# Kernel optimization log

Measured on AMD Instinct MI355X. Metric: run time of the kernel, lower is better.

The kernel has to match this reference:

```python
import jax, jax.numpy as jnp
import numpy as np

N_NODES = 100000
N_EDGES = 3200000
IN_F, HID, OUT = 3, 32, 1
NEG_SLOPE = 0.2


def _glorot(key, shape):
    fan_in, fan_out = shape[0], shape[-1]
    lim = jnp.sqrt(6.0 / (fan_in + fan_out)).astype(jnp.float32)
    return jax.random.uniform(key, shape, jnp.float32, -lim, lim)


def setup_inputs() -> dict:
    key = jax.random.key(0)
    ks = jax.random.split(key, 12)
    x = jax.random.normal(ks[0], (N_NODES, IN_F), jnp.float32)
    edge_index = jax.random.randint(ks[1], (2, N_EDGES), 0, N_NODES, jnp.int32)
    return {
        "x": x,
        "edge_index": edge_index,
        "W1": _glorot(ks[2], (IN_F, HID)),
        "att_src1": _glorot(ks[3], (1, HID))[0],
        "att_dst1": _glorot(ks[4], (1, HID))[0],
        "b1": jnp.zeros((HID,), jnp.float32),
        "W2": _glorot(ks[5], (HID, HID)),
        "att_src2": _glorot(ks[6], (1, HID))[0],
        "att_dst2": _glorot(ks[7], (1, HID))[0],
        "b2": jnp.zeros((HID,), jnp.float32),
        "Wl": _glorot(ks[8], (HID, OUT)),
        "bl": jnp.zeros((OUT,), jnp.float32),
    }


def gat_layer(x, src, dst, W, att_src, att_dst, b):
    # h: [N, HID] dense transform
    h = x @ W
    # per-node attention halves (compute once per node, gather per edge)
    a_s = h @ att_src  # [N]
    a_d = h @ att_dst  # [N]
    logits = jax.nn.leaky_relu(a_s[src] + a_d[dst], NEG_SLOPE)  # [E+N]
    # segment-softmax over incoming edges of each dst node
    m = jax.ops.segment_max(logits, dst, num_segments=N_NODES)
    m = jnp.where(jnp.isfinite(m), m, 0.0)
    ex = jnp.exp(logits - m[dst])
    denom = jax.ops.segment_sum(ex, dst, num_segments=N_NODES)
    coef = ex / (denom[dst] + 1e-16)
    # weighted scatter-aggregate of source messages
    out = jax.ops.segment_sum(coef[:, None] * h[src], dst, num_segments=N_NODES)
    return out + b


def reference(x, edge_index, W1, att_src1, att_dst1, b1, W2, att_src2, att_dst2, b2, Wl, bl):
    # PyG GATConv default: add self-loops
    loops = jnp.arange(N_NODES, dtype=edge_index.dtype)
    src = jnp.concatenate([edge_index[0], loops])
    dst = jnp.concatenate([edge_index[1], loops])
    h = gat_layer(x, src, dst, W1, att_src1, att_dst1, b1)
    h = jax.nn.relu(h)  # dropout is identity in eval
    h = gat_layer(h, src, dst, W2, att_src2, att_dst2, b2)
    h = jax.nn.relu(h)
    return h @ Wl + bl
```

## Files before the change

kernel.cpp:

```cpp
#include <hip/hip_runtime.h>
#include <hip/hip_fp16.h>

#define HID 32
#define BN 98
#define NBPAD 1024
#define BSTRIDE 3584
#define CHUNK 6144
#define EPT 12
#define CPAD 16

__device__ __forceinline__ float lrelu(float x) { return x > 0.0f ? x : 0.2f * x; }


__global__ void k_transform1(const float* __restrict__ x,
                             const float* __restrict__ W1,
                             const float* __restrict__ att_src,
                             const float* __restrict__ att_dst,
                             __half* __restrict__ hh,
                             float* __restrict__ a_s,
                             float* __restrict__ a_d,
                             int* __restrict__ cursor, int N)
{
    int tid = blockIdx.x * blockDim.x + threadIdx.x;
    if (tid < NBPAD * CPAD) cursor[tid] = 0;
    int n = tid >> 5, f = tid & 31;
    if (n >= N) return;
    float x0 = x[n * 3 + 0], x1 = x[n * 3 + 1], x2 = x[n * 3 + 2];
    float hv = x0 * W1[f] + x1 * W1[HID + f] + x2 * W1[2 * HID + f];
    hh[(size_t)n * HID + f] = __float2half(hv);
    float as = hv * att_src[f];
    float ad = hv * att_dst[f];
    #pragma unroll
    for (int m = 16; m >= 1; m >>= 1) {
        as += __shfl_xor(as, m, 32);
        ad += __shfl_xor(ad, m, 32);
    }
    if (f == 0) { a_s[n] = as; a_d[n] = ad; }
}


struct BinSM {
    int stage[CHUNK];
    unsigned short sbid[CHUNK];
    int lhist[NBPAD], lexcl[NBPAD], lbase[NBPAD], lcur[NBPAD];
    int arr[256];
};

__global__ void __launch_bounds__(512) k_binscatter(const int* __restrict__ src,
        const int* __restrict__ dst, int* __restrict__ cursor,
        unsigned int* __restrict__ packed, int NBr, int E)
{
    __shared__ BinSM S;
    int t = threadIdx.x;
    int base = blockIdx.x * CHUNK;
    int cnt = E - base; if (cnt > CHUNK) cnt = CHUNK;

    for (int i = t; i < NBPAD; i += 512) { S.lhist[i] = 0; S.lcur[i] = 0; }
    __syncthreads();

    int myd[EPT], mys[EPT];
    #pragma unroll
    for (int u = 0; u < EPT; ++u) {
        int i = t + u * 512;
        myd[u] = -1;
        if (i < cnt) {
            myd[u] = __builtin_nontemporal_load(&dst[base + i]);
            mys[u] = __builtin_nontemporal_load(&src[base + i]);
        }
    }
    #pragma unroll
    for (int u = 0; u < EPT; ++u)
        if (myd[u] >= 0) atomicAdd(&S.lhist[myd[u] / BN], 1);
    __syncthreads();

    int b0 = 4 * t;
    int c0 = 0, c1 = 0, c2 = 0, c3 = 0, s = 0;
    if (t < 256) {
        c0 = S.lhist[b0]; c1 = S.lhist[b0 + 1];
        c2 = S.lhist[b0 + 2]; c3 = S.lhist[b0 + 3];
        s = c0 + c1 + c2 + c3;
        S.arr[t] = s;
    }
    __syncthreads();
    for (int o = 1; o < 256; o <<= 1) {
        int v = (t < 256 && t >= o) ? S.arr[t - o] : 0;
        __syncthreads();
        if (t < 256) S.arr[t] += v;
        __syncthreads();
    }
    if (t < 256) {
        int ex = S.arr[t] - s;
        int e0 = ex, e1 = ex + c0, e2 = e1 + c1, e3 = e2 + c2;
        S.lexcl[b0] = e0; S.lexcl[b0 + 1] = e1;
        S.lexcl[b0 + 2] = e2; S.lexcl[b0 + 3] = e3;
        for (int i = 0; i < c0; ++i) S.sbid[e0 + i] = (unsigned short)b0;
        for (int i = 0; i < c1; ++i) S.sbid[e1 + i] = (unsigned short)(b0 + 1);
        for (int i = 0; i < c2; ++i) S.sbid[e2 + i] = (unsigned short)(b0 + 2);
        for (int i = 0; i < c3; ++i) S.sbid[e3 + i] = (unsigned short)(b0 + 3);
    }
    for (int b = t; b < NBr; b += 512)
        if (S.lhist[b])
            S.lbase[b] = b * BSTRIDE + atomicAdd(&cursor[b * CPAD], S.lhist[b]);
    __syncthreads();

    #pragma unroll
    for (int u = 0; u < EPT; ++u) {
        if (myd[u] >= 0) {
            int d = myd[u];
            int b = d / BN;
            int dl = d - b * BN;
            int idx = S.lexcl[b] + atomicAdd(&S.lcur[b], 1);
            S.stage[idx] = (int)((unsigned)mys[u] | ((unsigned)dl << 17));
        }
    }
    __syncthreads();

    for (int i = t; i < cnt; i += 512) {
        int b = S.sbid[i];
        int gpos = S.lbase[b] + (i - S.lexcl[b]);
        if (gpos < (b + 1) * BSTRIDE)
            __builtin_nontemporal_store((unsigned)S.stage[i], &packed[gpos]);
    }
}


struct AggSM {
    int2  lpair[BSTRIDE];
    int   lhist[256], lscan[256], lcur[256];
    float adT[BN];
};

__device__ __forceinline__ void build_csr(AggSM& S,
        const unsigned int* __restrict__ pk, int cnt,
        const float* __restrict__ a_s, const float* __restrict__ a_d,
        int nodeBase, int N)
{
    int t = threadIdx.x;
    if (t < 256) { S.lhist[t] = 0; S.lcur[t] = 0; }
    if (t < BN) { int n = nodeBase + t; S.adT[t] = (n < N) ? a_d[n] : 0.0f; }
    __syncthreads();
    unsigned myw[8];
    int mc = 0;
    for (int i = t; i < cnt; i += 512) {
        unsigned p = __builtin_nontemporal_load(&pk[i]);
        myw[mc++] = p;
        atomicAdd(&S.lhist[(p >> 17) & 255], 1);
    }
    __syncthreads();
    if (t < 256) S.lscan[t] = S.lhist[t];
    __syncthreads();
    for (int o = 1; o < 256; o <<= 1) {
        int v = (t < 256 && t >= o) ? S.lscan[t - o] : 0;
        __syncthreads();
        if (t < 256) S.lscan[t] += v;
        __syncthreads();
    }
    mc = 0;
    for (int i = t; i < cnt; i += 512) {
        unsigned p = myw[mc++];
        int dl = (p >> 17) & 255;
        int sv = (int)(p & 0x1FFFF);
        float e = __expf(lrelu(a_s[sv] + S.adT[dl]));
        int pos = atomicAdd(&S.lcur[dl], 1);
        S.lpair[(S.lscan[dl] - S.lhist[dl]) + pos] = make_int2(sv, __float_as_int(e));
    }
    __syncthreads();
}

__device__ __forceinline__ void agg_node(const __half* __restrict__ hh,
                                         float ex_self, const float* __restrict__ b,
                                         int n, int f,
                                         const int2* lpair,
                                         int off, int dg, float& vx, float& vy)
{
    float den = ex_self;
    float2 hs = __half22float2(*(const __half2*)(hh + (size_t)n * HID + 2 * f));
    float accx = ex_self * hs.x;
    float accy = ex_self * hs.y;
    int j = 0;
    for (; j + 8 <= dg; j += 8) {
        int2 p0 = lpair[off + j + 0], p1 = lpair[off + j + 1];
        int2 p2 = lpair[off + j + 2], p3 = lpair[off + j + 3];
        int2 p4 = lpair[off + j + 4], p5 = lpair[off + j + 5];
        int2 p6 = lpair[off + j + 6], p7 = lpair[off + j + 7];
        __half2 h0 = *(const __half2*)(hh + (size_t)p0.x * HID + 2 * f);
        __half2 h1 = *(const __half2*)(hh + (size_t)p1.x * HID + 2 * f);
        __half2 h2 = *(const __half2*)(hh + (size_t)p2.x * HID + 2 * f);
        __half2 h3 = *(const __half2*)(hh + (size_t)p3.x * HID + 2 * f);
        __half2 h4 = *(const __half2*)(hh + (size_t)p4.x * HID + 2 * f);
        __half2 h5 = *(const __half2*)(hh + (size_t)p5.x * HID + 2 * f);
        __half2 h6 = *(const __half2*)(hh + (size_t)p6.x * HID + 2 * f);
        __half2 h7 = *(const __half2*)(hh + (size_t)p7.x * HID + 2 * f);
        float e0 = __int_as_float(p0.y), e1 = __int_as_float(p1.y);
        float e2 = __int_as_float(p2.y), e3 = __int_as_float(p3.y);
        float e4 = __int_as_float(p4.y), e5 = __int_as_float(p5.y);
        float e6 = __int_as_float(p6.y), e7 = __int_as_float(p7.y);
        float2 q0 = __half22float2(h0), q1 = __half22float2(h1);
        float2 q2 = __half22float2(h2), q3 = __half22float2(h3);
        float2 q4 = __half22float2(h4), q5 = __half22float2(h5);
        float2 q6 = __half22float2(h6), q7 = __half22float2(h7);
        den += ((e0 + e1) + (e2 + e3)) + ((e4 + e5) + (e6 + e7));
        accx = fmaf(e0, q0.x, accx); accy = fmaf(e0, q0.y, accy);
        accx = fmaf(e1, q1.x, accx); accy = fmaf(e1, q1.y, accy);
        accx = fmaf(e2, q2.x, accx); accy = fmaf(e2, q2.y, accy);
        accx = fmaf(e3, q3.x, accx); accy = fmaf(e3, q3.y, accy);
        accx = fmaf(e4, q4.x, accx); accy = fmaf(e4, q4.y, accy);
        accx = fmaf(e5, q5.x, accx); accy = fmaf(e5, q5.y, accy);
        accx = fmaf(e6, q6.x, accx); accy = fmaf(e6, q6.y, accy);
        accx = fmaf(e7, q7.x, accx); accy = fmaf(e7, q7.y, accy);
    }
    for (; j < dg; ++j) {
        int2 p0 = lpair[off + j];
        float e0 = __int_as_float(p0.y);
        float2 q0 = __half22float2(*(const __half2*)(hh + (size_t)p0.x * HID + 2 * f));
        den += e0;
        accx = fmaf(e0, q0.x, accx);
        accy = fmaf(e0, q0.y, accy);
    }
    float inv = 1.0f / (den + 1e-16f);
    vx = fmaxf(accx * inv + b[2 * f], 0.0f);
    vy = fmaxf(accy * inv + b[2 * f + 1], 0.0f);
}

__device__ __forceinline__ void epi_mid(int n, int f, float vx, float vy,
        const float* __restrict__ W2, const float* __restrict__ as2w,
        const float* __restrict__ ad2w,
        __half* __restrict__ hh_out, float* __restrict__ as_out,
        float* __restrict__ ad_out)
{
    float hx = 0.0f, hy = 0.0f;
    #pragma unroll
    for (int k = 0; k < 16; ++k) {
        float va = __shfl(vx, k, 16);
        float vb = __shfl(vy, k, 16);
        float2 w0 = *(const float2*)(W2 + (2 * k) * HID + 2 * f);
        float2 w1 = *(const float2*)(W2 + (2 * k + 1) * HID + 2 * f);
        hx = fmaf(va, w0.x, hx); hy = fmaf(va, w0.y, hy);
        hx = fmaf(vb, w1.x, hx); hy = fmaf(vb, w1.y, hy);
    }
    *(__half2*)(hh_out + (size_t)n * HID + 2 * f) = __floats2half2_rn(hx, hy);
    float as = hx * as2w[2 * f] + hy * as2w[2 * f + 1];
    float ad = hx * ad2w[2 * f] + hy * ad2w[2 * f + 1];
    #pragma unroll
    for (int m2 = 8; m2 >= 1; m2 >>= 1) {
        as += __shfl_xor(as, m2, 16);
        ad += __shfl_xor(ad, m2, 16);
    }
    if (f == 0) { as_out[n] = as; ad_out[n] = ad; }
}


__global__ void __launch_bounds__(512, 8) k_agg_mid(const __half* __restrict__ hh,
        const float* __restrict__ a_s, const float* __restrict__ a_d,
        const int* __restrict__ cursor, const unsigned int* __restrict__ packed,
        const float* __restrict__ b1, const float* __restrict__ W2,
        const float* __restrict__ as2w, const float* __restrict__ ad2w,
        __half* __restrict__ hh_out, float* __restrict__ as_out,
        float* __restrict__ ad_out, int N)
{
    __shared__ AggSM S;
    int bk = blockIdx.x, t = threadIdx.x;
    int cnt = cursor[bk * CPAD]; if (cnt > BSTRIDE) cnt = BSTRIDE;
    build_csr(S, packed + (size_t)bk * BSTRIDE, cnt, a_s, a_d, bk * BN, N);
    int g = t >> 4, f = t & 15;
    for (int dl = g; dl < BN; dl += 32) {
        int n = bk * BN + dl;
        if (n >= N) continue;
        int off = S.lscan[dl] - S.lhist[dl];
        int dg = S.lhist[dl];
        float exs = __expf(lrelu(a_s[n] + S.adT[dl]));
        float vx, vy;
        agg_node(hh, exs, b1, n, f, S.lpair, off, dg, vx, vy);
        epi_mid(n, f, vx, vy, W2, as2w, ad2w, hh_out, as_out, ad_out);
    }
}

__global__ void __launch_bounds__(512, 8) k_agg_out(const __half* __restrict__ hh,
        const float* __restrict__ a_s, const float* __restrict__ a_d,
        const int* __restrict__ cursor, const unsigned int* __restrict__ packed,
        const float* __restrict__ b2, const float* __restrict__ Wl,
        const float* __restrict__ bl, float* __restrict__ out, int N)
{
    __shared__ AggSM S;
    int bk = blockIdx.x, t = threadIdx.x;
    int cnt = cursor[bk * CPAD]; if (cnt > BSTRIDE) cnt = BSTRIDE;
    build_csr(S, packed + (size_t)bk * BSTRIDE, cnt, a_s, a_d, bk * BN, N);
    int g = t >> 4, f = t & 15;
    for (int dl = g; dl < BN; dl += 32) {
        int n = bk * BN + dl;
        if (n >= N) continue;
        int off = S.lscan[dl] - S.lhist[dl];
        int dg = S.lhist[dl];
        float exs = __expf(lrelu(a_s[n] + S.adT[dl]));
        float vx, vy;
        agg_node(hh, exs, b2, n, f, S.lpair, off, dg, vx, vy);
        float y = vx * Wl[2 * f] + vy * Wl[2 * f + 1];
        #pragma unroll
        for (int m2 = 8; m2 >= 1; m2 >>= 1)
            y += __shfl_xor(y, m2, 16);
        if (f == 0) out[n] = y + bl[0];
    }
}


extern "C" void kernel_launch(void* const* d_in, const int* in_sizes, int n_in,
                              void* d_out, int out_size, void* d_ws, size_t ws_size,
                              hipStream_t stream)
{
    const float* x        = (const float*)d_in[0];
    const int*   eidx     = (const int*)d_in[1];
    const float* W1       = (const float*)d_in[2];
    const float* att_src1 = (const float*)d_in[3];
    const float* att_dst1 = (const float*)d_in[4];
    const float* b1       = (const float*)d_in[5];
    const float* W2       = (const float*)d_in[6];
    const float* att_src2 = (const float*)d_in[7];
    const float* att_dst2 = (const float*)d_in[8];
    const float* b2       = (const float*)d_in[9];
    const float* Wl       = (const float*)d_in[10];
    const float* bl       = (const float*)d_in[11];
    float* out = (float*)d_out;

    int N = in_sizes[0] / 3;
    int E = in_sizes[1] / 2;
    const int* src = eidx;
    const int* dst = eidx + E;
    int NBr = (N + BN - 1) / BN;

    size_t szNHh = (size_t)N * HID * 2;
    size_t szN4  = (size_t)N * 4;
    size_t szPK  = (size_t)NBr * BSTRIDE * 4;

    char* ws = (char*)d_ws;
    __half* h1h    = (__half*)ws; ws += szNHh;
    __half* h2h    = (__half*)ws; ws += szNHh;
    unsigned int* packed = (unsigned int*)ws; ws += szPK;
    float*  a_s1   = (float*)ws;  ws += szN4;
    float*  a_d1   = (float*)ws;  ws += szN4;
    float*  a_s2   = (float*)ws;  ws += szN4;
    float*  a_d2   = (float*)ws;  ws += szN4;
    int*    cursor = (int*)ws;    ws += (size_t)NBPAD * CPAD * 4;

    const int B = 256;
    int gridNode32 = (N * HID + B - 1) / B;
    int gridBin    = (E + CHUNK - 1) / CHUNK;

    k_transform1<<<gridNode32, B, 0, stream>>>(x, W1, att_src1, att_dst1,
                                               h1h, a_s1, a_d1, cursor, N);
    k_binscatter<<<gridBin, 512, 0, stream>>>(src, dst, cursor, packed, NBr, E);
    k_agg_mid<<<NBr, 512, 0, stream>>>(h1h, a_s1, a_d1, cursor, packed,
                                       b1, W2, att_src2, att_dst2,
                                       h2h, a_s2, a_d2, N);
    k_agg_out<<<NBr, 512, 0, stream>>>(h2h, a_s2, a_d2, cursor, packed,
                                       b2, Wl, bl, out, N);
}
```

Before: 270.0 us.

## Split node features into two half-width planes and gather each in separate passes

Node feature storage is split from one 32-wide fp16 row into two 16-wide planes (low and high feature halves). Aggregation now runs two passes over each node's edges, gathering 32 bytes per source from one plane at a time, so each pass touches a working set half the size, which is meant to fit better in cache. The cost is reading the edge list twice, plus scalar half loads in place of half2 loads. Separately, the nontemporal load/store hints in the bin scatter are dropped.

```diff
diff --git a/kernel.cpp b/kernel.cpp
--- a/kernel.cpp
+++ b/kernel.cpp
@@ -2,6 +2,7 @@
 #include <hip/hip_fp16.h>
 
 #define HID 32
+#define HHALF 16
 #define BN 98
 #define NBPAD 1024
 #define BSTRIDE 3584
@@ -16,7 +17,8 @@
                              const float* __restrict__ W1,
                              const float* __restrict__ att_src,
                              const float* __restrict__ att_dst,
-                             __half* __restrict__ hh,
+                             __half* __restrict__ h_lo,
+                             __half* __restrict__ h_hi,
                              float* __restrict__ a_s,
                              float* __restrict__ a_d,
                              int* __restrict__ cursor, int N)
@@ -27,7 +29,8 @@
     if (n >= N) return;
     float x0 = x[n * 3 + 0], x1 = x[n * 3 + 1], x2 = x[n * 3 + 2];
     float hv = x0 * W1[f] + x1 * W1[HID + f] + x2 * W1[2 * HID + f];
-    hh[(size_t)n * HID + f] = __float2half(hv);
+    if (f < HHALF) h_lo[(size_t)n * HHALF + f] = __float2half(hv);
+    else           h_hi[(size_t)n * HHALF + (f - HHALF)] = __float2half(hv);
     float as = hv * att_src[f];
     float ad = hv * att_dst[f];
     #pragma unroll
@@ -63,10 +66,7 @@
     for (int u = 0; u < EPT; ++u) {
         int i = t + u * 512;
         myd[u] = -1;
-        if (i < cnt) {
-            myd[u] = __builtin_nontemporal_load(&dst[base + i]);
-            mys[u] = __builtin_nontemporal_load(&src[base + i]);
-        }
+        if (i < cnt) { myd[u] = dst[base + i]; mys[u] = src[base + i]; }
     }
     #pragma unroll
     for (int u = 0; u < EPT; ++u)
@@ -119,7 +119,7 @@
         int b = S.sbid[i];
         int gpos = S.lbase[b] + (i - S.lexcl[b]);
         if (gpos < (b + 1) * BSTRIDE)
-            __builtin_nontemporal_store((unsigned)S.stage[i], &packed[gpos]);
+            packed[gpos] = (unsigned)S.stage[i];
     }
 }
 
@@ -167,80 +167,72 @@
     __syncthreads();
 }
 
-__device__ __forceinline__ void agg_node(const __half* __restrict__ hh,
-                                         float ex_self, const float* __restrict__ b,
-                                         int n, int f,
-                                         const int2* lpair,
-                                         int off, int dg, float& vx, float& vy)
-{
-    float den = ex_self;
-    float2 hs = __half22float2(*(const __half2*)(hh + (size_t)n * HID + 2 * f));
-    float accx = ex_self * hs.x;
-    float accy = ex_self * hs.y;
+template<bool WITH_DEN>
+__device__ __forceinline__ void agg_half(const __half* __restrict__ hh,
+        float exs, int n, int f, const int2* lpair, int off, int dg,
+        float& accOut, float& denOut)
+{
+    float den = exs;
+    float acc = exs * __half2float(hh[(size_t)n * HHALF + f]);
     int j = 0;
     for (; j + 8 <= dg; j += 8) {
         int2 p0 = lpair[off + j + 0], p1 = lpair[off + j + 1];
         int2 p2 = lpair[off + j + 2], p3 = lpair[off + j + 3];
         int2 p4 = lpair[off + j + 4], p5 = lpair[off + j + 5];
         int2 p6 = lpair[off + j + 6], p7 = lpair[off + j + 7];
-        __half2 h0 = *(const __half2*)(hh + (size_t)p0.x * HID + 2 * f);
-        __half2 h1 = *(const __half2*)(hh + (size_t)p1.x * HID + 2 * f);
-        __half2 h2 = *(const __half2*)(hh + (size_t)p2.x * HID + 2 * f);
-        __half2 h3 = *(const __half2*)(hh + (size_t)p3.x * HID + 2 * f);
-        __half2 h4 = *(const __half2*)(hh + (size_t)p4.x * HID + 2 * f);
-        __half2 h5 = *(const __half2*)(hh + (size_t)p5.x * HID + 2 * f);
-        __half2 h6 = *(const __half2*)(hh + (size_t)p6.x * HID + 2 * f);
-        __half2 h7 = *(const __half2*)(hh + (size_t)p7.x * HID + 2 * f);
+        __half v0 = hh[(size_t)p0.x * HHALF + f];
+        __half v1 = hh[(size_t)p1.x * HHALF + f];
+        __half v2 = hh[(size_t)p2.x * HHALF + f];
+        __half v3 = hh[(size_t)p3.x * HHALF + f];
+        __half v4 = hh[(size_t)p4.x * HHALF + f];
+        __half v5 = hh[(size_t)p5.x * HHALF + f];
+        __half v6 = hh[(size_t)p6.x * HHALF + f];
+        __half v7 = hh[(size_t)p7.x * HHALF + f];
         float e0 = __int_as_float(p0.y), e1 = __int_as_float(p1.y);
         float e2 = __int_as_float(p2.y), e3 = __int_as_float(p3.y);
         float e4 = __int_as_float(p4.y), e5 = __int_as_float(p5.y);
         float e6 = __int_as_float(p6.y), e7 = __int_as_float(p7.y);
-        float2 q0 = __half22float2(h0), q1 = __half22float2(h1);
-        float2 q2 = __half22float2(h2), q3 = __half22float2(h3);
-        float2 q4 = __half22float2(h4), q5 = __half22float2(h5);
-        float2 q6 = __half22float2(h6), q7 = __half22float2(h7);
-        den += ((e0 + e1) + (e2 + e3)) + ((e4 + e5) + (e6 + e7));
-        accx = fmaf(e0, q0.x, accx); accy = fmaf(e0, q0.y, accy);
-        accx = fmaf(e1, q1.x, accx); accy = fmaf(e1, q1.y, accy);
-        accx = fmaf(e2, q2.x, accx); accy = fmaf(e2, q2.y, accy);
-        accx = fmaf(e3, q3.x, accx); accy = fmaf(e3, q3.y, accy);
-        accx = fmaf(e4, q4.x, accx); accy = fmaf(e4, q4.y, accy);
-        accx = fmaf(e5, q5.x, accx); accy = fmaf(e5, q5.y, accy);
-        accx = fmaf(e6, q6.x, accx); accy = fmaf(e6, q6.y, accy);
-        accx = fmaf(e7, q7.x, accx); accy = fmaf(e7, q7.y, accy);
+        if (WITH_DEN)
+            den += ((e0 + e1) + (e2 + e3)) + ((e4 + e5) + (e6 + e7));
+        acc = fmaf(e0, __half2float(v0), acc);
+        acc = fmaf(e1, __half2float(v1), acc);
+        acc = fmaf(e2, __half2float(v2), acc);
+        acc = fmaf(e3, __half2float(v3), acc);
+        acc = fmaf(e4, __half2float(v4), acc);
+        acc = fmaf(e5, __half2float(v5), acc);
+        acc = fmaf(e6, __half2float(v6), acc);
+        acc = fmaf(e7, __half2float(v7), acc);
     }
     for (; j < dg; ++j) {
-        int2 p0 = lpair[off + j];
-        float e0 = __int_as_float(p0.y);
-        float2 q0 = __half22float2(*(const __half2*)(hh + (size_t)p0.x * HID + 2 * f));
-        den += e0;
-        accx = fmaf(e0, q0.x, accx);
-        accy = fmaf(e0, q0.y, accy);
-    }
-    float inv = 1.0f / (den + 1e-16f);
-    vx = fmaxf(accx * inv + b[2 * f], 0.0f);
-    vy = fmaxf(accy * inv + b[2 * f + 1], 0.0f);
+        int2 pp = lpair[off + j];
+        float e = __int_as_float(pp.y);
+        if (WITH_DEN) den += e;
+        acc = fmaf(e, __half2float(hh[(size_t)pp.x * HHALF + f]), acc);
+    }
+    accOut = acc;
+    if (WITH_DEN) denOut = den;
 }
 
 __device__ __forceinline__ void epi_mid(int n, int f, float vx, float vy,
         const float* __restrict__ W2, const float* __restrict__ as2w,
         const float* __restrict__ ad2w,
-        __half* __restrict__ hh_out, float* __restrict__ as_out,
-        float* __restrict__ ad_out)
+        __half* __restrict__ h2_lo, __half* __restrict__ h2_hi,
+        float* __restrict__ as_out, float* __restrict__ ad_out)
 {
     float hx = 0.0f, hy = 0.0f;
     #pragma unroll
     for (int k = 0; k < 16; ++k) {
         float va = __shfl(vx, k, 16);
         float vb = __shfl(vy, k, 16);
-        float2 w0 = *(const float2*)(W2 + (2 * k) * HID + 2 * f);
-        float2 w1 = *(const float2*)(W2 + (2 * k + 1) * HID + 2 * f);
-        hx = fmaf(va, w0.x, hx); hy = fmaf(va, w0.y, hy);
-        hx = fmaf(vb, w1.x, hx); hy = fmaf(vb, w1.y, hy);
-    }
-    *(__half2*)(hh_out + (size_t)n * HID + 2 * f) = __floats2half2_rn(hx, hy);
-    float as = hx * as2w[2 * f] + hy * as2w[2 * f + 1];
-    float ad = hx * ad2w[2 * f] + hy * ad2w[2 * f + 1];
+        hx = fmaf(va, W2[k * HID + f], hx);
+        hy = fmaf(va, W2[k * HID + HHALF + f], hy);
+        hx = fmaf(vb, W2[(k + HHALF) * HID + f], hx);
+        hy = fmaf(vb, W2[(k + HHALF) * HID + HHALF + f], hy);
+    }
+    h2_lo[(size_t)n * HHALF + f] = __float2half(hx);
+    h2_hi[(size_t)n * HHALF + f] = __float2half(hy);
+    float as = hx * as2w[f] + hy * as2w[HHALF + f];
+    float ad = hx * ad2w[f] + hy * ad2w[HHALF + f];
     #pragma unroll
     for (int m2 = 8; m2 >= 1; m2 >>= 1) {
         as += __shfl_xor(as, m2, 16);
@@ -250,32 +242,66 @@
 }
 
 
-__global__ void __launch_bounds__(512, 8) k_agg_mid(const __half* __restrict__ hh,
+__global__ void __launch_bounds__(512, 8) k_agg_mid(
+        const __half* __restrict__ h_lo, const __half* __restrict__ h_hi,
         const float* __restrict__ a_s, const float* __restrict__ a_d,
         const int* __restrict__ cursor, const unsigned int* __restrict__ packed,
         const float* __restrict__ b1, const float* __restrict__ W2,
         const float* __restrict__ as2w, const float* __restrict__ ad2w,
-        __half* __restrict__ hh_out, float* __restrict__ as_out,
-        float* __restrict__ ad_out, int N)
+        __half* __restrict__ h2_lo, __half* __restrict__ h2_hi,
+        float* __restrict__ as_out, float* __restrict__ ad_out, int N)
 {
     __shared__ AggSM S;
     int bk = blockIdx.x, t = threadIdx.x;
     int cnt = cursor[bk * CPAD]; if (cnt > BSTRIDE) cnt = BSTRIDE;
     build_csr(S, packed + (size_t)bk * BSTRIDE, cnt, a_s, a_d, bk * BN, N);
     int g = t >> 4, f = t & 15;
-    for (int dl = g; dl < BN; dl += 32) {
-        int n = bk * BN + dl;
+    int nb = bk * BN;
+    float den[4], alo[4], ahi[4];
+    #pragma unroll
+    for (int i = 0; i < 4; ++i) {
+        int dl = g + 32 * i;
+        den[i] = 1.0f; alo[i] = 0.0f;
+        if (dl < BN) {
+            int n = nb + dl;
+            if (n < N) {
+                int off = S.lscan[dl] - S.lhist[dl];
+                int dg = S.lhist[dl];
+                float exs = __expf(lrelu(a_s[n] + S.adT[dl]));
+                agg_half<true>(h_lo, exs, n, f, S.lpair, off, dg, alo[i], den[i]);
+            }
+        }
+    }
+    #pragma unroll
+    for (int i = 0; i < 4; ++i) {
+        int dl = g + 32 * i;
+        ahi[i] = 0.0f;
+        if (dl < BN) {
+            int n = nb + dl;
+            if (n < N) {
+                int off = S.lscan[dl] - S.lhist[dl];
+                int dg = S.lhist[dl];
+                float exs = __expf(lrelu(a_s[n] + S.adT[dl]));
+                float dummy;
+                agg_half<false>(h_hi, exs, n, f, S.lpair, off, dg, ahi[i], dummy);
+            }
+        }
+    }
+    #pragma unroll
+    for (int i = 0; i < 4; ++i) {
+        int dl = g + 32 * i;
+        if (dl >= BN) continue;
+        int n = nb + dl;
         if (n >= N) continue;
-        int off = S.lscan[dl] - S.lhist[dl];
-        int dg = S.lhist[dl];
-        float exs = __expf(lrelu(a_s[n] + S.adT[dl]));
-        float vx, vy;
-        agg_node(hh, exs, b1, n, f, S.lpair, off, dg, vx, vy);
-        epi_mid(n, f, vx, vy, W2, as2w, ad2w, hh_out, as_out, ad_out);
-    }
-}
-
-__global__ void __launch_bounds__(512, 8) k_agg_out(const __half* __restrict__ hh,
+        float inv = 1.0f / (den[i] + 1e-16f);
+        float vx = fmaxf(alo[i] * inv + b1[f], 0.0f);
+        float vy = fmaxf(ahi[i] * inv + b1[HHALF + f], 0.0f);
+        epi_mid(n, f, vx, vy, W2, as2w, ad2w, h2_lo, h2_hi, as_out, ad_out);
+    }
+}
+
+__global__ void __launch_bounds__(512, 8) k_agg_out(
+        const __half* __restrict__ h_lo, const __half* __restrict__ h_hi,
         const float* __restrict__ a_s, const float* __restrict__ a_d,
         const int* __restrict__ cursor, const unsigned int* __restrict__ packed,
         const float* __restrict__ b2, const float* __restrict__ Wl,
@@ -286,15 +312,47 @@
     int cnt = cursor[bk * CPAD]; if (cnt > BSTRIDE) cnt = BSTRIDE;
     build_csr(S, packed + (size_t)bk * BSTRIDE, cnt, a_s, a_d, bk * BN, N);
     int g = t >> 4, f = t & 15;
-    for (int dl = g; dl < BN; dl += 32) {
-        int n = bk * BN + dl;
+    int nb = bk * BN;
+    float den[4], alo[4], ahi[4];
+    #pragma unroll
+    for (int i = 0; i < 4; ++i) {
+        int dl = g + 32 * i;
+        den[i] = 1.0f; alo[i] = 0.0f;
+        if (dl < BN) {
+            int n = nb + dl;
+            if (n < N) {
+                int off = S.lscan[dl] - S.lhist[dl];
+                int dg = S.lhist[dl];
+                float exs = __expf(lrelu(a_s[n] + S.adT[dl]));
+                agg_half<true>(h_lo, exs, n, f, S.lpair, off, dg, alo[i], den[i]);
+            }
+        }
+    }
+    #pragma unroll
+    for (int i = 0; i < 4; ++i) {
+        int dl = g + 32 * i;
+        ahi[i] = 0.0f;
+        if (dl < BN) {
+            int n = nb + dl;
+            if (n < N) {
+                int off = S.lscan[dl] - S.lhist[dl];
+                int dg = S.lhist[dl];
+                float exs = __expf(lrelu(a_s[n] + S.adT[dl]));
+                float dummy;
+                agg_half<false>(h_hi, exs, n, f, S.lpair, off, dg, ahi[i], dummy);
+            }
+        }
+    }
+    #pragma unroll
+    for (int i = 0; i < 4; ++i) {
+        int dl = g + 32 * i;
+        if (dl >= BN) continue;
+        int n = nb + dl;
         if (n >= N) continue;
-        int off = S.lscan[dl] - S.lhist[dl];
-        int dg = S.lhist[dl];
-        float exs = __expf(lrelu(a_s[n] + S.adT[dl]));
-        float vx, vy;
-        agg_node(hh, exs, b2, n, f, S.lpair, off, dg, vx, vy);
-        float y = vx * Wl[2 * f] + vy * Wl[2 * f + 1];
+        float inv = 1.0f / (den[i] + 1e-16f);
+        float vx = fmaxf(alo[i] * inv + b2[f], 0.0f);
+        float vy = fmaxf(ahi[i] * inv + b2[HHALF + f], 0.0f);
+        float y = vx * Wl[f] + vy * Wl[HHALF + f];
         #pragma unroll
         for (int m2 = 8; m2 >= 1; m2 >>= 1)
             y += __shfl_xor(y, m2, 16);
@@ -327,13 +385,15 @@
     const int* dst = eidx + E;
     int NBr = (N + BN - 1) / BN;
 
-    size_t szNHh = (size_t)N * HID * 2;
+    size_t szNHalf = (size_t)N * HHALF * 2;
     size_t szN4  = (size_t)N * 4;
     size_t szPK  = (size_t)NBr * BSTRIDE * 4;
 
     char* ws = (char*)d_ws;
-    __half* h1h    = (__half*)ws; ws += szNHh;
-    __half* h2h    = (__half*)ws; ws += szNHh;
+    __half* h1_lo  = (__half*)ws; ws += szNHalf;
+    __half* h1_hi  = (__half*)ws; ws += szNHalf;
+    __half* h2_lo  = (__half*)ws; ws += szNHalf;
+    __half* h2_hi  = (__half*)ws; ws += szNHalf;
     unsigned int* packed = (unsigned int*)ws; ws += szPK;
     float*  a_s1   = (float*)ws;  ws += szN4;
     float*  a_d1   = (float*)ws;  ws += szN4;
@@ -346,11 +406,11 @@
     int gridBin    = (E + CHUNK - 1) / CHUNK;
 
     k_transform1<<<gridNode32, B, 0, stream>>>(x, W1, att_src1, att_dst1,
-                                               h1h, a_s1, a_d1, cursor, N);
+                                               h1_lo, h1_hi, a_s1, a_d1, cursor, N);
     k_binscatter<<<gridBin, 512, 0, stream>>>(src, dst, cursor, packed, NBr, E);
-    k_agg_mid<<<NBr, 512, 0, stream>>>(h1h, a_s1, a_d1, cursor, packed,
+    k_agg_mid<<<NBr, 512, 0, stream>>>(h1_lo, h1_hi, a_s1, a_d1, cursor, packed,
                                        b1, W2, att_src2, att_dst2,
-                                       h2h, a_s2, a_d2, N);
-    k_agg_out<<<NBr, 512, 0, stream>>>(h2h, a_s2, a_d2, cursor, packed,
+                                       h2_lo, h2_hi, a_s2, a_d2, N);
+    k_agg_out<<<NBr, 512, 0, stream>>>(h2_lo, h2_hi, a_s2, a_d2, cursor, packed,
                                        b2, Wl, bl, out, N);
 }
```

Measured after the change: 295.4 us. 9.4% more time.
